# Performance work log

Measured on AMD Instinct MI355X. Metric: run time of the kernel, lower is better.

Reference implementation:

```python
import jax, jax.numpy as jnp
import numpy as np

B_SZ = 4; SEQ = 2048; D_INPUT = 40; D_MODEL = 128; N_LAYERS = 4
D_STATE = 16; EXPAND = 2; D_INNER = D_MODEL * EXPAND
N_HEADS = 4; D_HEAD = D_MODEL // N_HEADS; MAX_LANDMARKS = 100
EPS_RMS = 1.1920929e-07  # torch nn.RMSNorm default eps = finfo(float32).eps
EPS_LN = 1e-5
A_FLOOR = 1e-4


def _rms(x, w):
    return x * jax.lax.rsqrt(jnp.mean(x * x, -1, keepdims=True) + EPS_RMS) * w


def _ln(x, w, b):
    m = jnp.mean(x, -1, keepdims=True)
    v = jnp.mean((x - m) ** 2, -1, keepdims=True)
    return (x - m) * jax.lax.rsqrt(v + EPS_LN) * w + b


def _mamba3_block(xin, Wi, Wx, Wdt, bdt, Alog, Bb, Cb, Bnw, Cnw, rf, Dv, Wo):
    # xin: (B,L,d_model)
    xz = xin @ Wi                       # (B,L,2*d_inner)
    xp, z = jnp.split(xz, 2, axis=-1)
    xp = jax.nn.silu(xp)
    sp = xp @ Wx                        # (B,L,2*d_state+2)
    B_raw = sp[..., :D_STATE]
    C_raw = sp[..., D_STATE:2 * D_STATE]
    dt_in = sp[..., -2:-1]
    lam_in = sp[..., -1:]
    Bm = _rms(B_raw + Bb, Bnw)
    Cm = _rms(C_raw + Cb, Cnw)
    dt = jax.nn.softplus(dt_in @ Wdt + bdt)   # (B,L,d_inner)
    lam = jax.nn.sigmoid(lam_in)              # (B,L,1)
    # data-dependent RoPE on B and C
    freqs = jax.nn.softplus(rf)                                  # (d_state//2,)
    ang = jnp.cumsum(jnp.mean(dt, -1, keepdims=True), axis=1) * freqs  # (B,L,ds/2)
    ca, sa = jnp.cos(ang), jnp.sin(ang)

    def rot(M):
        e, o = M[..., ::2], M[..., 1::2]
        return jnp.stack([e * ca - o * sa, e * sa + o * ca], -1).reshape(M.shape)

    Bm, Cm = rot(Bm), rot(Cm)
    A = jnp.minimum(-jnp.exp(Alog), -A_FLOOR)   # (d_inner,d_state)
    dte = dt[..., None]                          # (B,L,d_inner,1)
    dA = jnp.exp(A * dte)                        # (B,L,d_inner,d_state)
    Bx = Bm[:, :, None, :] * xp[..., None]       # (B,L,d_inner,d_state)
    Bx_prev = jnp.concatenate([jnp.zeros_like(Bx[:, :1]), Bx[:, :-1]], axis=1)
    lame = lam[..., None]                        # (B,L,1,1)
    u = (1.0 - lame) * dte * dA * Bx_prev + lame * dte * Bx
    u = u.at[:, 0].set(dte[:, 0] * Bx[:, 0])     # t==0 case: h = dt*B*x (no lambda)

    def step(h, inp):
        dA_t, u_t, C_t = inp
        h = dA_t * h + u_t
        return h, jnp.sum(h * C_t[:, None, :], -1)

    h0 = jnp.zeros((xin.shape[0], D_INNER, D_STATE), xin.dtype)
    _, ys = jax.lax.scan(step, h0, (jnp.swapaxes(dA, 0, 1), jnp.swapaxes(u, 0, 1), jnp.swapaxes(Cm, 0, 1)))
    y = jnp.swapaxes(ys, 0, 1)                   # (B,L,d_inner)
    y = y + xp * Dv
    y = y * jax.nn.silu(z)
    return y @ Wo


def _landmark_attn(mo, skip, hw, WQ, bQ, WK, bK, WV, bV, WO, bO):
    Bsz, L, Dm = skip.shape
    k = min(MAX_LANDMARKS, L)
    _, idx = jax.lax.top_k(hw, k)
    idx = jnp.sort(idx, axis=1)                            # (B,k)
    kv = jnp.take_along_axis(skip, idx[..., None], axis=1)  # (B,k,Dm)
    q = mo[:, -1:, :]                                       # (B,1,Dm)
    Q = (q @ WQ + bQ).reshape(Bsz, 1, N_HEADS, D_HEAD).transpose(0, 2, 1, 3)
    K = (kv @ WK + bK).reshape(Bsz, k, N_HEADS, D_HEAD).transpose(0, 2, 1, 3)
    V = (kv @ WV + bV).reshape(Bsz, k, N_HEADS, D_HEAD).transpose(0, 2, 1, 3)
    scores = jnp.einsum('bhqd,bhkd->bhqk', Q, K) * (D_HEAD ** -0.5)
    probs = jax.nn.softmax(scores, axis=-1)
    out = jnp.einsum('bhqk,bhkd->bhqd', probs, V).transpose(0, 2, 1, 3).reshape(Bsz, Dm)
    return out @ WO + bO


def setup_inputs() -> dict:
    key = jax.random.key(0)
    ks = iter(jax.random.split(key, 64))

    def nrm(shape, s=0.02):
        return jax.random.normal(next(ks), shape, jnp.float32) * s

    nl, ds, di, dm = N_LAYERS, D_STATE, D_INNER, D_MODEL
    inp = {}
    inp['x'] = jax.random.normal(next(ks), (B_SZ, SEQ, D_INPUT), jnp.float32)
    inp['hawkes_weights'] = jax.random.uniform(next(ks), (B_SZ, SEQ), jnp.float32)
    inp['emb_W'] = nrm((D_INPUT, dm)); inp['emb_b'] = jnp.zeros(dm, jnp.float32)
    inp['skip_W'] = nrm((D_INPUT, dm)); inp['skip_b'] = jnp.zeros(dm, jnp.float32)
    inp['in_proj_W'] = nrm((nl, dm, 2 * di))
    inp['x_proj_W'] = nrm((nl, di, 2 * ds + 2))
    inp['dt_proj_W'] = nrm((nl, 1, di), 1.0)
    inp['dt_proj_b'] = jnp.full((nl, di), -1.0, jnp.float32)
    inp['A_log'] = jnp.broadcast_to(jnp.log(jnp.arange(1, ds + 1, dtype=jnp.float32)), (nl, di, ds)) * jnp.ones((nl, di, ds), jnp.float32)
    inp['B_bias'] = jnp.ones((nl, ds), jnp.float32)
    inp['C_bias'] = jnp.ones((nl, ds), jnp.float32)
    inp['Bn_w'] = jnp.ones((nl, ds), jnp.float32)
    inp['Cn_w'] = jnp.ones((nl, ds), jnp.float32)
    inp['rope_freqs'] = nrm((nl, ds // 2), 0.01)
    inp['D_param'] = jnp.ones((nl, di), jnp.float32)
    inp['out_proj_W'] = nrm((nl, di, dm))
    inp['ln_w'] = jnp.ones((nl, dm), jnp.float32); inp['ln_b'] = jnp.zeros((nl, dm), jnp.float32)
    inp['fn_w'] = jnp.ones(dm, jnp.float32); inp['fn_b'] = jnp.zeros(dm, jnp.float32)
    for nm in ('Q', 'K', 'V', 'O'):
        inp['W' + nm] = nrm((dm, dm)); inp['b' + nm] = jnp.zeros(dm, jnp.float32)
    return inp


def reference(x, hawkes_weights, emb_W, emb_b, skip_W, skip_b, in_proj_W, x_proj_W,
              dt_proj_W, dt_proj_b, A_log, B_bias, C_bias, Bn_w, Cn_w, rope_freqs,
              D_param, out_proj_W, ln_w, ln_b, fn_w, fn_b, WQ, bQ, WK, bK, WV, bV, WO, bO):
    w = hawkes_weights[..., None]
    h = (x @ emb_W + emb_b) * w          # Hawkes-damped embedding for Mamba path
    skip = (x @ skip_W + skip_b) * w     # Hawkes skip for attention KV
    for i in range(N_LAYERS):
        h = h + _mamba3_block(_ln(h, ln_w[i], ln_b[i]), in_proj_W[i], x_proj_W[i],
                              dt_proj_W[i], dt_proj_b[i], A_log[i], B_bias[i], C_bias[i],
                              Bn_w[i], Cn_w[i], rope_freqs[i], D_param[i], out_proj_W[i])
    mo = _ln(h, fn_w, fn_b)
    return _landmark_attn(mo, skip, hawkes_weights, WQ, bQ, WK, bK, WV, bV, WO, bO)
```

## Files before the change

kernel.cpp:

```cpp
#include <hip/hip_runtime.h>
#include <hip/hip_fp16.h>
#include <math.h>

#define BSZ   4
#define SEQL  2048
#define DIN   40
#define DM    128
#define DI    256
#define DS    16
#define NL    4
#define NHEAD 4
#define DHEAD 32
#define KLM   100
#define NC    128
#define TC    16
#define NROWS 8
#define EROWS 16

__device__ __forceinline__ float rcp_(float x){ return __builtin_amdgcn_rcpf(x); }
__device__ __forceinline__ float sigmoidf_(float x){ return rcp_(1.0f + __expf(-x)); }
__device__ __forceinline__ float siluf_(float x){ return x*rcp_(1.0f + __expf(-x)); }
__device__ __forceinline__ float softplusf_(float x){ return fmaxf(x,0.0f) + __logf(1.0f + __expf(-fabsf(x))); }

__device__ __forceinline__ float block_sum256(float v, float* red){
  #pragma unroll
  for (int o=32;o>0;o>>=1) v += __shfl_down(v,o,64);
  __syncthreads();
  if ((threadIdx.x & 63)==0) red[threadIdx.x>>6] = v;
  __syncthreads();
  return red[0]+red[1]+red[2]+red[3];
}
__device__ __forceinline__ void load8(const float* p, float* r){
  const float4* q = (const float4*)p;
  float4 a=q[0], b=q[1];
  r[0]=a.x;r[1]=a.y;r[2]=a.z;r[3]=a.w; r[4]=b.x;r[5]=b.y;r[6]=b.z;r[7]=b.w;
}
__device__ __forceinline__ void store8(float* p, const float* r){
  float4* q = (float4*)p;
  q[0]=make_float4(r[0],r[1],r[2],r[3]);  q[1]=make_float4(r[4],r[5],r[6],r[7]);
}
__device__ __forceinline__ void load16(const float* p, float* r){
  load8(p, r); load8(p+8, r+8);
}
__device__ __forceinline__ void store16(float* p, const float* r){
  store8(p, r); store8(p+8, r+8);
}

__global__ __launch_bounds__(256) void embed_kernel(
    const float* __restrict__ x, const float* __restrict__ hw,
    const float* __restrict__ eW, const float* __restrict__ eb,
    const float* __restrict__ sW, const float* __restrict__ sb,
    float* __restrict__ hb, float* __restrict__ sk)
{
  __shared__ float xr[EROWS][DIN];
  const int t = threadIdx.x;
  const size_t R0 = (size_t)blockIdx.x * EROWS;
  for (int e=t; e<EROWS*DIN; e+=256) ((float*)xr)[e] = x[R0*DIN + e];
  __syncthreads();
  const int c = t & (DM-1), g = t >> 7;
  float ae[8], as[8];
  #pragma unroll
  for (int j=0;j<8;j++){ ae[j]=0.0f; as[j]=0.0f; }
  for (int k=0;k<DIN;k++){
    const float we  = eW[(size_t)k*DM + c];
    const float ws_ = sW[(size_t)k*DM + c];
    #pragma unroll
    for (int j=0;j<8;j++){
      const float xv = xr[g*8+j][k];
      ae[j] = fmaf(xv, we, ae[j]);
      as[j] = fmaf(xv, ws_, as[j]);
    }
  }
  const float ebv = eb[c], sbv = sb[c];
  #pragma unroll
  for (int j=0;j<8;j++){
    const size_t R = R0 + g*8 + j;
    const float w = hw[R];
    hb[R*DM + c] = (ae[j]+ebv)*w;
    sk[R*DM + c] = (as[j]+sbv)*w;
  }
}

__global__ __launch_bounds__(256) void pre_kernel(
    const float* __restrict__ hb,
    const float* __restrict__ Wi, const float* __restrict__ Wx,
    const float* __restrict__ Wdt, const float* __restrict__ bdt,
    const float* __restrict__ Bb, const float* __restrict__ Cb,
    const float* __restrict__ Bnw, const float* __restrict__ Cnw,
    const float* __restrict__ lnw, const float* __restrict__ lnb,
    __half* __restrict__ xph, __half* __restrict__ zsh,
    float* __restrict__ dtin, float* __restrict__ Shalf,
    float* __restrict__ Bmb, float* __restrict__ Cmb,
    float* __restrict__ lamb, float* __restrict__ mdtb)
{
  __shared__ float xin[NROWS][DM+4];
  __shared__ float xps[NROWS][DI+4];
  __shared__ float spl[NROWS][40];
  __shared__ float pr[NROWS][4];

  const int t = threadIdx.x;
  const size_t R0 = (size_t)blockIdx.x * NROWS;

  {
    const int r = t >> 5, j = t & 31;
    const float4 v = ((const float4*)(hb + (R0 + r)*DM))[j];
    float s = v.x+v.y+v.z+v.w;
    #pragma unroll
    for (int o=16;o>0;o>>=1) s += __shfl_xor(s,o,32);
    const float m = s*(1.0f/DM);
    const float dx=v.x-m, dy=v.y-m, dz=v.z-m, dw=v.w-m;
    float ss = dx*dx+dy*dy+dz*dz+dw*dw;
    #pragma unroll
    for (int o=16;o>0;o>>=1) ss += __shfl_xor(ss,o,32);
    const float inv = 1.0f/sqrtf(ss*(1.0f/DM) + 1e-5f);
    const int c = j*4;
    xin[r][c+0] = dx*inv*lnw[c+0] + lnb[c+0];
    xin[r][c+1] = dy*inv*lnw[c+1] + lnb[c+1];
    xin[r][c+2] = dz*inv*lnw[c+2] + lnb[c+2];
    xin[r][c+3] = dw*inv*lnw[c+3] + lnb[c+3];
  }
  __syncthreads();

  {
    float2 a[NROWS];
    #pragma unroll
    for (int r=0;r<NROWS;r++){ a[r].x=0.0f; a[r].y=0.0f; }
    for (int k=0;k<DM;k+=4){
      const float2 w0 = *(const float2*)&Wi[(size_t)(k+0)*(2*DI) + 2*t];
      const float2 w1 = *(const float2*)&Wi[(size_t)(k+1)*(2*DI) + 2*t];
      const float2 w2 = *(const float2*)&Wi[(size_t)(k+2)*(2*DI) + 2*t];
      const float2 w3 = *(const float2*)&Wi[(size_t)(k+3)*(2*DI) + 2*t];
      #pragma unroll
      for (int r=0;r<NROWS;r++){
        const float4 xv = *(const float4*)&xin[r][k];
        a[r].x = fmaf(xv.x,w0.x,a[r].x); a[r].y = fmaf(xv.x,w0.y,a[r].y);
        a[r].x = fmaf(xv.y,w1.x,a[r].x); a[r].y = fmaf(xv.y,w1.y,a[r].y);
        a[r].x = fmaf(xv.z,w2.x,a[r].x); a[r].y = fmaf(xv.z,w2.y,a[r].y);
        a[r].x = fmaf(xv.w,w3.x,a[r].x); a[r].y = fmaf(xv.w,w3.y,a[r].y);
      }
    }
    if (t < 128){
      #pragma unroll
      for (int r=0;r<NROWS;r++){
        const float sx = siluf_(a[r].x), sy = siluf_(a[r].y);
        xps[r][2*t] = sx; xps[r][2*t+1] = sy;
        *(__half2*)&xph[(R0+r)*DI + 2*t] =
            __halves2half2(__float2half_rn(sx), __float2half_rn(sy));
      }
    } else {
      const int zc = 2*t - 2*DI + DI;
      #pragma unroll
      for (int r=0;r<NROWS;r++){
        const float sx = siluf_(a[r].x), sy = siluf_(a[r].y);
        *(__half2*)&zsh[(R0+r)*DI + zc] =
            __halves2half2(__float2half_rn(sx), __float2half_rn(sy));
      }
    }
  }
  __syncthreads();

  if (t < 136){
    const int r = t & 7, op = t >> 3;
    float ax=0.0f, ay=0.0f;
    for (int k=0;k<DI;k+=4){
      const float4 xv = *(const float4*)&xps[r][k];
      const float2 w0 = *(const float2*)&Wx[(size_t)(k+0)*34 + 2*op];
      const float2 w1 = *(const float2*)&Wx[(size_t)(k+1)*34 + 2*op];
      const float2 w2 = *(const float2*)&Wx[(size_t)(k+2)*34 + 2*op];
      const float2 w3 = *(const float2*)&Wx[(size_t)(k+3)*34 + 2*op];
      ax = fmaf(xv.x,w0.x,ax); ay = fmaf(xv.x,w0.y,ay);
      ax = fmaf(xv.y,w1.x,ax); ay = fmaf(xv.y,w1.y,ay);
      ax = fmaf(xv.z,w2.x,ax); ay = fmaf(xv.z,w2.y,ay);
      ax = fmaf(xv.w,w3.x,ax); ay = fmaf(xv.w,w3.y,ay);
    }
    spl[r][2*op] = ax; spl[r][2*op+1] = ay;
  }
  __syncthreads();

  {
    const int half = t >> 7;
    const int r2 = (t >> 4) & 7, s2 = t & 15;
    const float* bias = half ? Cb : Bb;
    const float* wn   = half ? Cnw : Bnw;
    const float v = spl[r2][half*DS + s2] + bias[s2];
    float ss = v*v;
    #pragma unroll
    for (int o=8;o>0;o>>=1) ss += __shfl_xor(ss,o,16);
    const float inv = 1.0f/sqrtf(ss*(1.0f/DS) + 1.1920929e-07f);
    (half ? Cmb : Bmb)[(R0+r2)*DS + s2] = v*inv*wn[s2];
  }

  {
    const int lane = t & 63, w = t >> 6;
    const float wdt = Wdt[t], bdtv = bdt[t];
    float Sd = 0.0f;
    #pragma unroll
    for (int r=0;r<NROWS;r++){
      const float dval = softplusf_(fmaf(spl[r][32], wdt, bdtv));
      Sd += dval;
      float s = dval;
      #pragma unroll
      for (int o=32;o>0;o>>=1) s += __shfl_xor(s,o,64);
      if (lane==0) pr[r][w] = s;
    }
    Shalf[(size_t)blockIdx.x * DI + t] = Sd;
    if (t < NROWS){
      lamb[R0+t] = sigmoidf_(spl[t][33]);
      dtin[R0+t] = spl[t][32];
    }
  }
  __syncthreads();
  if (t < NROWS)
    mdtb[R0+t] = (pr[t][0]+pr[t][1]+pr[t][2]+pr[t][3])*(1.0f/DI);
}

__global__ __launch_bounds__(256) void cumsum_kernel(
    const float* __restrict__ mdt, double* __restrict__ csum_g)
{
  __shared__ double wsum[4];
  const int b = blockIdx.x, t = threadIdx.x;
  const int lane = t & 63, w = t >> 6;
  const float* p = mdt + (size_t)b*SEQL + (size_t)t*8;
  double v[8]; double s = 0.0;
  #pragma unroll
  for (int q=0;q<8;q++){ v[q] = (double)p[q]; s += v[q]; }
  double sc = s;
  #pragma unroll
  for (int o=1;o<64;o<<=1){
    const double nb = __shfl_up(sc, o, 64);
    if (lane >= o) sc += nb;
  }
  if (lane==63) wsum[w] = sc;
  __syncthreads();
  double woff = 0.0;
  for (int j=0;j<w;j++) woff += wsum[j];
  double run = woff + sc - s;
  double* dst = csum_g + (size_t)b*SEQL + (size_t)t*8;
  #pragma unroll
  for (int q=0;q<8;q++){ run += v[q]; dst[q] = run; }
}

__global__ __launch_bounds__(256) void csfill_kernel(
    const double* __restrict__ csum_g, const float* __restrict__ rf,
    float2* __restrict__ cst)
{
  __shared__ double fqs[8];
  const int t = threadIdx.x;
  if (t < 8){
    const double xfr = (double)rf[t];
    fqs[t] = fmax(xfr, 0.0) + log1p(exp(-fabs(xfr)));
  }
  __syncthreads();
  const int row = blockIdx.x*256 + t;
  const double ab = csum_g[row];
  const double TWO_PI = 6.283185307179586;
  const double INV2PI = 0.15915494309189535;
  float2 o8[8];
  #pragma unroll
  for (int f=0; f<8; f++){
    const double ang = ab * fqs[f];
    const double red = ang - floor(ang*INV2PI)*TWO_PI;
    float sa, ca;
    __sincosf((float)red, &sa, &ca);
    o8[f] = make_float2(ca, sa);
  }
  float4* dst = (float4*)&cst[(size_t)row*8];
  dst[0] = make_float4(o8[0].x,o8[0].y,o8[1].x,o8[1].y);
  dst[1] = make_float4(o8[2].x,o8[2].y,o8[3].x,o8[3].y);
  dst[2] = make_float4(o8[4].x,o8[4].y,o8[5].x,o8[5].y);
  dst[3] = make_float4(o8[6].x,o8[6].y,o8[7].x,o8[7].y);
}

__global__ __launch_bounds__(512) void scan1_kernel(
    const __half* __restrict__ xph, const float* __restrict__ dtin,
    const float* __restrict__ Wdt, const float* __restrict__ bdt,
    const float* __restrict__ Bmb, const float* __restrict__ lamb,
    const float2* __restrict__ cst,
    const float* __restrict__ Alog, float* __restrict__ hend)
{
  __shared__ float Bst[TC+1][DS];
  __shared__ float lst[TC];
  __shared__ float dsl[TC];
  __shared__ __half xpl[TC+1][DI+8];
  const int t = threadIdx.x;
  const int d  = t >> 1;
  const int s0 = (t & 1) * 8;
  const int c = blockIdx.x & (NC-1);
  const int b = blockIdx.x >> 7;
  const size_t bL = (size_t)b*SEQL;
  const int t0 = c*TC;
  const int id = blockIdx.x*256 + d;

  for (int e=t; e<(TC+1)*DS; e+=512){
    const int j = e >> 4, s = e & 15;
    const int trow = t0 - 1 + j;
    Bst[j][s] = (trow >= 0) ? Bmb[(bL + trow)*DS + s] : 0.0f;
  }
  for (int e=t; e<(TC+1)*DI; e+=512){
    const int j = e >> 8, dd = e & (DI-1);
    const int trow = t0 - 1 + j;
    xpl[j][dd] = (trow >= 0) ? xph[(bL + trow)*DI + dd] : __float2half_rn(0.0f);
  }
  if (t < TC){
    lst[t] = lamb[bL + t0 + t];
    dsl[t] = dtin[bL + t0 + t];
  }
  __syncthreads();
  if (t < 136){
    const int j = t >> 3, f = t & 7;
    const int trow = t0 - 1 + j;
    if (trow >= 0){
      const float2 cs = cst[((size_t)(bL + trow))*8 + f];
      const float e0 = Bst[j][2*f], o0 = Bst[j][2*f+1];
      Bst[j][2*f]   = e0*cs.x - o0*cs.y;
      Bst[j][2*f+1] = e0*cs.y + o0*cs.x;
    }
  }
  __syncthreads();

  float A[8];
  #pragma unroll
  for (int s=0;s<8;s++) A[s] = fminf(-__expf(Alog[d*DS + s0 + s]), -1e-4f);
  const float wdt = Wdt[d], bdtv = bdt[d];
  float h[8], Bprev[8];
  #pragma unroll
  for (int s=0;s<8;s++) h[s]=0.0f;
  float xpm1;
  int tstart;
  if (t0 > 0){
    #pragma unroll
    for (int s=0;s<8;s++) Bprev[s] = Bst[0][s0+s];
    xpm1 = __half2float(xpl[0][d]);
    tstart = t0;
  } else {
    const float dtv = softplusf_(fmaf(dsl[0], wdt, bdtv));
    const float xpv = __half2float(xpl[1][d]);
    #pragma unroll
    for (int s=0;s<8;s++){
      h[s] = dtv*(Bst[1][s0+s]*xpv);
      Bprev[s] = Bst[1][s0+s];
    }
    xpm1 = xpv;
    tstart = 1;
  }
  for (int tt=tstart; tt<t0+TC; ++tt){
    const int j = tt - t0;
    const float dtv = softplusf_(fmaf(dsl[j], wdt, bdtv));
    const float xpv = __half2float(xpl[j+1][d]);
    const float lamv = lst[j];
    const float dl = dtv*lamv;
    const float dml = dtv - dl;
    #pragma unroll
    for (int s=0;s<8;s++){
      const float a = __expf(A[s]*dtv);
      const float Bc = Bst[j+1][s0+s];
      const float u = fmaf(dml*a, Bprev[s]*xpm1, dl*(Bc*xpv));
      h[s] = fmaf(a, h[s], u);
      Bprev[s] = Bc;
    }
    xpm1 = xpv;
  }
  store8(hend + (size_t)id*DS + s0, h);
}

__global__ __launch_bounds__(128) void scan2_kernel(
    float* __restrict__ hend, const float* __restrict__ Shalf,
    const float* __restrict__ Alog)
{
  __shared__ float hS[NC][DS+1];
  __shared__ float pS[NC][DS+1];
  const int c = threadIdx.x;
  const int d = blockIdx.x & (DI-1);
  const int b = blockIdx.x >> 8;
  const float S = Shalf[(size_t)(b*(SEQL/NROWS) + 2*c)*DI + d]
                + Shalf[(size_t)(b*(SEQL/NROWS) + 2*c + 1)*DI + d];
  float P[DS], h[DS];
  #pragma unroll
  for (int s=0;s<DS;s++){
    const float A = fminf(-__expf(Alog[d*DS+s]), -1e-4f);
    P[s] = __expf(A*S);
  }
  load16(hend + (((size_t)(b*NC + c))*DI + d)*DS, h);
  #pragma unroll
  for (int s=0;s<DS;s++){ hS[c][s]=h[s]; pS[c][s]=P[s]; }
  __syncthreads();
  for (int off=1; off<NC; off<<=1){
    float hn[DS], pn[DS];
    const int src = c - off;
    if (src >= 0){
      #pragma unroll
      for (int s=0;s<DS;s++){ hn[s]=hS[src][s]; pn[s]=pS[src][s]; }
    }
    __syncthreads();
    if (src >= 0){
      #pragma unroll
      for (int s=0;s<DS;s++){
        h[s] = fmaf(P[s], hn[s], h[s]);
        P[s] *= pn[s];
        hS[c][s] = h[s]; pS[c][s] = P[s];
      }
    }
    __syncthreads();
  }
  float o[DS];
  if (c == 0){
    #pragma unroll
    for (int s=0;s<DS;s++) o[s] = 0.0f;
  } else {
    #pragma unroll
    for (int s=0;s<DS;s++) o[s] = hS[c-1][s];
  }
  store16(hend + (((size_t)(b*NC + c))*DI + d)*DS, o);
}

__global__ __launch_bounds__(512) void scan3post_kernel(
    const __half* __restrict__ xph, const float* __restrict__ dtin,
    const float* __restrict__ Wdt, const float* __restrict__ bdt,
    const float* __restrict__ Bmb, const float* __restrict__ Cmb,
    const float* __restrict__ lamb, const __half* __restrict__ zsh,
    const float2* __restrict__ cst,
    const float* __restrict__ Alog, const float* __restrict__ Dv,
    const float* __restrict__ Hin, const float* __restrict__ Wo,
    float* __restrict__ hb)
{
  __shared__ float Bst[TC+1][DS];
  __shared__ float Cst[TC][DS];
  __shared__ float lst[TC];
  __shared__ float dsl[TC];
  __shared__ __half xpl[TC+1][DI+8];
  __shared__ __half zsl[TC][DI+8];
  __shared__ float ys[TC][DI+4];
  const int t = threadIdx.x;
  const int d  = t >> 1;
  const int sh = t & 1;
  const int s0 = sh * 8;
  const int c = blockIdx.x & (NC-1);
  const int b = blockIdx.x >> 7;
  const size_t bL = (size_t)b*SEQL;
  const int t0 = c*TC;
  const int id = blockIdx.x*256 + d;

  for (int e=t; e<(TC+1)*DS; e+=512){
    const int j = e >> 4, s = e & 15;
    const int trow = t0 - 1 + j;
    Bst[j][s] = (trow >= 0) ? Bmb[(bL + trow)*DS + s] : 0.0f;
    if (j < TC) Cst[j][s] = Cmb[(bL + t0 + j)*DS + s];
  }
  for (int e=t; e<(TC+1)*DI; e+=512){
    const int j = e >> 8, dd = e & (DI-1);
    const int trow = t0 - 1 + j;
    xpl[j][dd] = (trow >= 0) ? xph[(bL + trow)*DI + dd] : __float2half_rn(0.0f);
    if (j < TC) zsl[j][dd] = zsh[(bL + t0 + j)*DI + dd];
  }
  if (t < TC){
    lst[t] = lamb[bL + t0 + t];
    dsl[t] = dtin[bL + t0 + t];
  }
  __syncthreads();
  if (t < 264){
    if (t < 136){
      const int j = t >> 3, f = t & 7;
      const int trow = t0 - 1 + j;
      if (trow >= 0){
        const float2 cs = cst[((size_t)(bL + trow))*8 + f];
        const float e0 = Bst[j][2*f], o0 = Bst[j][2*f+1];
        Bst[j][2*f]   = e0*cs.x - o0*cs.y;
        Bst[j][2*f+1] = e0*cs.y + o0*cs.x;
      }
    } else {
      const int e2 = t - 136;
      const int j = e2 >> 3, f = e2 & 7;
      const float2 cs = cst[((size_t)(bL + t0 + j))*8 + f];
      const float e0 = Cst[j][2*f], o0 = Cst[j][2*f+1];
      Cst[j][2*f]   = e0*cs.x - o0*cs.y;
      Cst[j][2*f+1] = e0*cs.y + o0*cs.x;
    }
  }
  __syncthreads();

  float A[8];
  #pragma unroll
  for (int s=0;s<8;s++) A[s] = fminf(-__expf(Alog[d*DS + s0 + s]), -1e-4f);
  const float wdt = Wdt[d], bdtv = bdt[d];
  const float dvp = Dv[d];
  float h[8], Bprev[8];
  load8(Hin + (size_t)id*DS + s0, h);
  float xpm1;
  int tstart;
  if (t0 > 0){
    #pragma unroll
    for (int s=0;s<8;s++) Bprev[s] = Bst[0][s0+s];
    xpm1 = __half2float(xpl[0][d]);
    tstart = t0;
  } else {
    const float dtv = softplusf_(fmaf(dsl[0], wdt, bdtv));
    const float xpv = __half2float(xpl[1][d]);
    float y = 0.0f;
    #pragma unroll
    for (int s=0;s<8;s++){
      h[s] = dtv*(Bst[1][s0+s]*xpv);
      y = fmaf(h[s], Cst[0][s0+s], y);
      Bprev[s] = Bst[1][s0+s];
    }
    const float ytot = y + __shfl_xor(y, 1, 64);
    if (sh == 0) ys[0][d] = (ytot + xpv*dvp)*__half2float(zsl[0][d]);
    xpm1 = xpv;
    tstart = 1;
  }
  for (int tt=tstart; tt<t0+TC; ++tt){
    const int j = tt - t0;
    const float dtv = softplusf_(fmaf(dsl[j], wdt, bdtv));
    const float xpv = __half2float(xpl[j+1][d]);
    const float lamv = lst[j];
    const float dl = dtv*lamv;
    const float dml = dtv - dl;
    float y = 0.0f;
    #pragma unroll
    for (int s=0;s<8;s++){
      const float a = __expf(A[s]*dtv);
      const float Bc = Bst[j+1][s0+s];
      const float u = fmaf(dml*a, Bprev[s]*xpm1, dl*(Bc*xpv));
      h[s] = fmaf(a, h[s], u);
      y = fmaf(h[s], Cst[j][s0+s], y);
      Bprev[s] = Bc;
    }
    const float ytot = y + __shfl_xor(y, 1, 64);
    if (sh == 0) ys[j][d] = (ytot + xpv*dvp)*__half2float(zsl[j][d]);
    xpm1 = xpv;
  }
  __syncthreads();

  {
    const int r  = t >> 5;
    const int cg = t & 31;
    const int c0 = cg*4;
    float acc[4] = {0.0f,0.0f,0.0f,0.0f};
    for (int k=0;k<DI;k+=4){
      const float4 yv = *(const float4*)&ys[r][k];
      const float yy[4] = {yv.x, yv.y, yv.z, yv.w};
      #pragma unroll
      for (int j=0;j<4;j++){
        const float4 wa = *(const float4*)&Wo[(size_t)(k+j)*DM + c0];
        acc[0]=fmaf(yy[j],wa.x,acc[0]); acc[1]=fmaf(yy[j],wa.y,acc[1]);
        acc[2]=fmaf(yy[j],wa.z,acc[2]); acc[3]=fmaf(yy[j],wa.w,acc[3]);
      }
    }
    const size_t row = bL + t0 + r;
    float4 h0 = *(const float4*)&hb[row*DM + c0];
    h0.x+=acc[0]; h0.y+=acc[1]; h0.z+=acc[2]; h0.w+=acc[3];
    *(float4*)&hb[row*DM + c0] = h0;
  }
}

__global__ __launch_bounds__(256) void topk_kernel(
    const float* __restrict__ hb, const float* __restrict__ hw,
    const float* __restrict__ fnw, const float* __restrict__ fnb,
    int* __restrict__ idxl_g, float* __restrict__ mog)
{
  __shared__ int redcnt[2][4];
  __shared__ int eqc[8][4], gtc[8][4];
  __shared__ float red_f[4];

  const int b = blockIdx.x;
  const int t = threadIdx.x;
  const int lane = t & 63, w = t >> 6;

  const float* hwp = hw + (size_t)b*SEQL;
  unsigned vb[8];
  #pragma unroll
  for (int q=0;q<8;q++) vb[q] = __float_as_uint(hwp[q*256 + t]);

  unsigned kth = 0u;
  for (int bit=31; bit>=0; --bit){
    const unsigned cand = kth | (1u << bit);
    int c0 = 0;
    #pragma unroll
    for (int q=0;q<8;q++) c0 += __popcll(__ballot(vb[q] >= cand));
    const int par = bit & 1;
    if (lane == 0) redcnt[par][w] = c0;
    __syncthreads();
    const int tot = redcnt[par][0]+redcnt[par][1]+redcnt[par][2]+redcnt[par][3];
    if (tot >= KLM) kth = cand;
  }

  unsigned long long beq[8], bgt[8];
  #pragma unroll
  for (int q=0;q<8;q++){
    beq[q] = __ballot(vb[q] == kth);
    bgt[q] = __ballot(vb[q] >  kth);
  }
  if (lane == 0){
    #pragma unroll
    for (int q=0;q<8;q++){ eqc[q][w] = __popcll(beq[q]); gtc[q][w] = __popcll(bgt[q]); }
  }
  __syncthreads();
  {
    int gtTot = 0;
    #pragma unroll
    for (int q=0;q<8;q++) gtTot += gtc[q][0]+gtc[q][1]+gtc[q][2]+gtc[q][3];
    const int need_eq = KLM - gtTot;
    const unsigned long long lmask = (lane==0) ? 0ull : ((~0ull) >> (64-lane));
    int eqPfx = 0, gtPfx = 0;
    #pragma unroll
    for (int q=0;q<8;q++){
      int eqWP = 0, gtWP = 0;
      for (int w2=0; w2<w; ++w2){ eqWP += eqc[q][w2]; gtWP += gtc[q][w2]; }
      const int eqBefore = eqPfx + eqWP + __popcll(beq[q] & lmask);
      const int gtBefore = gtPfx + gtWP + __popcll(bgt[q] & lmask);
      if (vb[q] > kth){
        const int pos = gtBefore + min(eqBefore, need_eq);
        if (pos < KLM) idxl_g[b*KLM + pos] = q*256 + t;
      } else if (vb[q] == kth && eqBefore < need_eq){
        const int pos = gtBefore + eqBefore;
        if (pos < KLM) idxl_g[b*KLM + pos] = q*256 + t;
      }
      eqPfx += eqc[q][0]+eqc[q][1]+eqc[q][2]+eqc[q][3];
      gtPfx += gtc[q][0]+gtc[q][1]+gtc[q][2]+gtc[q][3];
    }
  }

  {
    const float* hr = hb + ((size_t)b*SEQL + (SEQL-1))*DM;
    const float hv = (t < DM) ? hr[t] : 0.0f;
    const float ssum = block_sum256(hv, red_f);
    const float mean = ssum*(1.0f/DM);
    const float dv = (t < DM) ? (hv - mean) : 0.0f;
    const float vsum = block_sum256(dv*dv, red_f);
    const float inv = 1.0f/sqrtf(vsum*(1.0f/DM) + 1e-5f);
    if (t < DM) mog[b*DM + t] = dv*inv*fnw[t] + fnb[t];
  }
}

__global__ __launch_bounds__(256) void attnmid_kernel(
    const float* __restrict__ sk, const int* __restrict__ idxl_g,
    const float* __restrict__ mog,
    const float* __restrict__ WQ, const float* __restrict__ bQ,
    const float* __restrict__ WK, const float* __restrict__ bK,
    const float* __restrict__ WV, const float* __restrict__ bV,
    float* __restrict__ attnog)
{
  __shared__ float kv[KLM][DM+4];
  __shared__ float Qs[DHEAD];
  __shared__ float qk[DM];
  __shared__ float sc[KLM];
  __shared__ float pbar[DM];
  __shared__ float bterm_s;
  const int t = threadIdx.x;
  const int b = blockIdx.x >> 2, hh = blockIdx.x & 3;
  const int c0 = hh*DHEAD;

  for (int e=t; e<KLM*DM; e+=256){
    const int j = e >> 7, cc = e & (DM-1);
    kv[j][cc] = sk[((size_t)b*SEQL + idxl_g[b*KLM + j])*DM + cc];
  }
  if (t < DHEAD){
    float a = bQ[c0+t];
    #pragma unroll 4
    for (int k=0;k<DM;k++) a = fmaf(mog[b*DM+k], WQ[(size_t)k*DM + c0+t], a);
    Qs[t] = a;
  }
  __syncthreads();
  if (t < DM){
    float a = 0.0f;
    #pragma unroll
    for (int cc=0; cc<DHEAD; cc++) a = fmaf(WK[(size_t)t*DM + c0 + cc], Qs[cc], a);
    qk[t] = a;
  } else if (t == DM){
    float a = 0.0f;
    for (int cc=0; cc<DHEAD; cc++) a += bK[c0+cc]*Qs[cc];
    bterm_s = a;
  }
  __syncthreads();
  if (t < KLM){
    float a = bterm_s;
    for (int m=0;m<DM;m+=4){
      const float4 kvv = *(const float4*)&kv[t][m];
      const float4 qv  = *(const float4*)&qk[m];
      a = fmaf(kvv.x,qv.x,a); a = fmaf(kvv.y,qv.y,a);
      a = fmaf(kvv.z,qv.z,a); a = fmaf(kvv.w,qv.w,a);
    }
    sc[t] = a*0.17677669529663687f;
  }
  __syncthreads();
  if (t < 64){
    const int lane = t;
    const float v0 = (lane < KLM) ? sc[lane] : -3.0e38f;
    const float v1 = (lane+64 < KLM) ? sc[lane+64] : -3.0e38f;
    float mx = fmaxf(v0, v1);
    #pragma unroll
    for (int o2=32;o2>0;o2>>=1) mx = fmaxf(mx, __shfl_xor(mx,o2,64));
    const float e0 = (lane < KLM) ? __expf(v0-mx) : 0.0f;
    const float e1 = (lane+64 < KLM) ? __expf(v1-mx) : 0.0f;
    float sm = e0+e1;
    #pragma unroll
    for (int o2=32;o2>0;o2>>=1) sm += __shfl_xor(sm,o2,64);
    const float inv2 = rcp_(sm);
    if (lane < KLM) sc[lane] = e0*inv2;
    if (lane+64 < KLM) sc[lane+64] = e1*inv2;
  }
  __syncthreads();
  if (t < DM){
    float a = 0.0f;
    #pragma unroll 4
    for (int j=0;j<KLM;j++) a = fmaf(sc[j], kv[j][t], a);
    pbar[t] = a;
  }
  __syncthreads();
  if (t < DHEAD){
    const int cc = c0 + t;
    float a = bV[cc];
    #pragma unroll 4
    for (int m=0;m<DM;m++) a = fmaf(pbar[m], WV[(size_t)m*DM + cc], a);
    attnog[b*DM + cc] = a;
  }
}

__global__ __launch_bounds__(128) void attnout_kernel(
    const float* __restrict__ attnog, const float* __restrict__ WO,
    const float* __restrict__ bO, float* __restrict__ outp)
{
  __shared__ float ao[DM];
  const int b = blockIdx.x, t = threadIdx.x;
  ao[t] = attnog[b*DM + t];
  __syncthreads();
  float a = bO[t];
  #pragma unroll 4
  for (int c2=0;c2<DM;c2++) a = fmaf(ao[c2], WO[(size_t)c2*DM + t], a);
  outp[(size_t)b*DM + t] = a;
}

extern "C" void kernel_launch(void* const* d_in, const int* in_sizes, int n_in,
                              void* d_out, int out_size, void* d_ws, size_t ws_size,
                              hipStream_t stream)
{
  (void)in_sizes; (void)n_in; (void)out_size; (void)ws_size;
  const float* x    = (const float*)d_in[0];
  const float* hw   = (const float*)d_in[1];
  const float* embW = (const float*)d_in[2];
  const float* embB = (const float*)d_in[3];
  const float* skW  = (const float*)d_in[4];
  const float* skB  = (const float*)d_in[5];
  const float* inW  = (const float*)d_in[6];
  const float* xpW  = (const float*)d_in[7];
  const float* dtW  = (const float*)d_in[8];
  const float* dtB  = (const float*)d_in[9];
  const float* Alog = (const float*)d_in[10];
  const float* Bb   = (const float*)d_in[11];
  const float* Cb   = (const float*)d_in[12];
  const float* Bnw  = (const float*)d_in[13];
  const float* Cnw  = (const float*)d_in[14];
  const float* rf   = (const float*)d_in[15];
  const float* Dpar = (const float*)d_in[16];
  const float* outW = (const float*)d_in[17];
  const float* lnW  = (const float*)d_in[18];
  const float* lnB  = (const float*)d_in[19];
  const float* fnW  = (const float*)d_in[20];
  const float* fnB  = (const float*)d_in[21];
  const float* WQ = (const float*)d_in[22]; const float* bQ = (const float*)d_in[23];
  const float* WK = (const float*)d_in[24]; const float* bK = (const float*)d_in[25];
  const float* WV = (const float*)d_in[26]; const float* bV = (const float*)d_in[27];
  const float* WO = (const float*)d_in[28]; const float* bO = (const float*)d_in[29];

  float* ws = (float*)d_ws;
  size_t off = 0;
  float* hb    = ws + off; off += (size_t)BSZ*SEQL*DM;
  float* sk    = ws + off; off += (size_t)BSZ*SEQL*DM;
  __half* xph  = (__half*)(ws + off); off += (size_t)BSZ*SEQL*DI/2;
  __half* zsh  = (__half*)(ws + off); off += (size_t)BSZ*SEQL*DI/2;
  float* Bmb   = ws + off; off += (size_t)BSZ*SEQL*DS;
  float* Cmb   = ws + off; off += (size_t)BSZ*SEQL*DS;
  float* lamb  = ws + off; off += (size_t)BSZ*SEQL;
  float* mdtb  = ws + off; off += (size_t)BSZ*SEQL;
  float* dtin  = ws + off; off += (size_t)BSZ*SEQL;
  float* Shalf = ws + off; off += (size_t)BSZ*(SEQL/NROWS)*DI;
  float* hend  = ws + off; off += (size_t)BSZ*NC*DI*DS;
  float2* cst  = (float2*)(ws + off); off += (size_t)BSZ*SEQL*16;
  double* csum_g = (double*)(ws + off); off += (size_t)BSZ*SEQL*2;
  int* idxl_g  = (int*)(ws + off); off += (size_t)BSZ*KLM;
  float* mog   = ws + off; off += (size_t)BSZ*DM;
  float* attnog= ws + off; off += (size_t)BSZ*DM;

  embed_kernel<<<BSZ*SEQL/EROWS, 256, 0, stream>>>(x, hw, embW, embB, skW, skB, hb, sk);

  for (int i=0;i<NL;i++){
    pre_kernel<<<BSZ*SEQL/NROWS, 256, 0, stream>>>(hb,
        inW + (size_t)i*DM*2*DI, xpW + (size_t)i*DI*34,
        dtW + (size_t)i*DI, dtB + (size_t)i*DI,
        Bb + i*DS, Cb + i*DS, Bnw + i*DS, Cnw + i*DS,
        lnW + i*DM, lnB + i*DM,
        xph, zsh, dtin, Shalf, Bmb, Cmb, lamb, mdtb);
    cumsum_kernel<<<BSZ, 256, 0, stream>>>(mdtb, csum_g);
    csfill_kernel<<<BSZ*SEQL/256, 256, 0, stream>>>(csum_g, rf + i*8, cst);
    scan1_kernel<<<BSZ*NC, 512, 0, stream>>>(xph, dtin,
        dtW + (size_t)i*DI, dtB + (size_t)i*DI,
        Bmb, lamb, cst, Alog + (size_t)i*DI*DS, hend);
    scan2_kernel<<<BSZ*DI, 128, 0, stream>>>(hend, Shalf, Alog + (size_t)i*DI*DS);
    scan3post_kernel<<<BSZ*NC, 512, 0, stream>>>(xph, dtin,
        dtW + (size_t)i*DI, dtB + (size_t)i*DI,
        Bmb, Cmb, lamb, zsh, cst,
        Alog + (size_t)i*DI*DS, Dpar + (size_t)i*DI, hend,
        outW + (size_t)i*DI*DM, hb);
  }

  topk_kernel<<<BSZ, 256, 0, stream>>>(hb, hw, fnW, fnB, idxl_g, mog);
  attnmid_kernel<<<BSZ*NHEAD, 256, 0, stream>>>(sk, idxl_g, mog,
      WQ, bQ, WK, bK, WV, bV, attnog);
  attnout_kernel<<<BSZ, 128, 0, stream>>>(attnog, WO, bO, (float*)d_out);
}
```

Before: 576.3 us.

## Fuse chunked scan passes into one cooperative kernel with grid syncs

```diff
diff --git a/kernel.cpp b/kernel.cpp
--- a/kernel.cpp
+++ b/kernel.cpp
@@ -1,6 +1,9 @@
 #include <hip/hip_runtime.h>
 #include <hip/hip_fp16.h>
+#include <hip/hip_cooperative_groups.h>
 #include <math.h>
+
+namespace cg = cooperative_groups;
 
 #define BSZ   4
 #define SEQL  2048
@@ -38,12 +41,6 @@
 __device__ __forceinline__ void store8(float* p, const float* r){
   float4* q = (float4*)p;
   q[0]=make_float4(r[0],r[1],r[2],r[3]);  q[1]=make_float4(r[4],r[5],r[6],r[7]);
-}
-__device__ __forceinline__ void load16(const float* p, float* r){
-  load8(p, r); load8(p+8, r+8);
-}
-__device__ __forceinline__ void store16(float* p, const float* r){
-  store8(p, r); store8(p+8, r+8);
 }
 
 __global__ __launch_bounds__(256) void embed_kernel(
@@ -271,157 +268,15 @@
   dst[3] = make_float4(o8[6].x,o8[6].y,o8[7].x,o8[7].y);
 }
 
-__global__ __launch_bounds__(512) void scan1_kernel(
-    const __half* __restrict__ xph, const float* __restrict__ dtin,
-    const float* __restrict__ Wdt, const float* __restrict__ bdt,
-    const float* __restrict__ Bmb, const float* __restrict__ lamb,
-    const float2* __restrict__ cst,
-    const float* __restrict__ Alog, float* __restrict__ hend)
-{
-  __shared__ float Bst[TC+1][DS];
-  __shared__ float lst[TC];
-  __shared__ float dsl[TC];
-  __shared__ __half xpl[TC+1][DI+8];
-  const int t = threadIdx.x;
-  const int d  = t >> 1;
-  const int s0 = (t & 1) * 8;
-  const int c = blockIdx.x & (NC-1);
-  const int b = blockIdx.x >> 7;
-  const size_t bL = (size_t)b*SEQL;
-  const int t0 = c*TC;
-  const int id = blockIdx.x*256 + d;
-
-  for (int e=t; e<(TC+1)*DS; e+=512){
-    const int j = e >> 4, s = e & 15;
-    const int trow = t0 - 1 + j;
-    Bst[j][s] = (trow >= 0) ? Bmb[(bL + trow)*DS + s] : 0.0f;
-  }
-  for (int e=t; e<(TC+1)*DI; e+=512){
-    const int j = e >> 8, dd = e & (DI-1);
-    const int trow = t0 - 1 + j;
-    xpl[j][dd] = (trow >= 0) ? xph[(bL + trow)*DI + dd] : __float2half_rn(0.0f);
-  }
-  if (t < TC){
-    lst[t] = lamb[bL + t0 + t];
-    dsl[t] = dtin[bL + t0 + t];
-  }
-  __syncthreads();
-  if (t < 136){
-    const int j = t >> 3, f = t & 7;
-    const int trow = t0 - 1 + j;
-    if (trow >= 0){
-      const float2 cs = cst[((size_t)(bL + trow))*8 + f];
-      const float e0 = Bst[j][2*f], o0 = Bst[j][2*f+1];
-      Bst[j][2*f]   = e0*cs.x - o0*cs.y;
-      Bst[j][2*f+1] = e0*cs.y + o0*cs.x;
-    }
-  }
-  __syncthreads();
-
-  float A[8];
-  #pragma unroll
-  for (int s=0;s<8;s++) A[s] = fminf(-__expf(Alog[d*DS + s0 + s]), -1e-4f);
-  const float wdt = Wdt[d], bdtv = bdt[d];
-  float h[8], Bprev[8];
-  #pragma unroll
-  for (int s=0;s<8;s++) h[s]=0.0f;
-  float xpm1;
-  int tstart;
-  if (t0 > 0){
-    #pragma unroll
-    for (int s=0;s<8;s++) Bprev[s] = Bst[0][s0+s];
-    xpm1 = __half2float(xpl[0][d]);
-    tstart = t0;
-  } else {
-    const float dtv = softplusf_(fmaf(dsl[0], wdt, bdtv));
-    const float xpv = __half2float(xpl[1][d]);
-    #pragma unroll
-    for (int s=0;s<8;s++){
-      h[s] = dtv*(Bst[1][s0+s]*xpv);
-      Bprev[s] = Bst[1][s0+s];
-    }
-    xpm1 = xpv;
-    tstart = 1;
-  }
-  for (int tt=tstart; tt<t0+TC; ++tt){
-    const int j = tt - t0;
-    const float dtv = softplusf_(fmaf(dsl[j], wdt, bdtv));
-    const float xpv = __half2float(xpl[j+1][d]);
-    const float lamv = lst[j];
-    const float dl = dtv*lamv;
-    const float dml = dtv - dl;
-    #pragma unroll
-    for (int s=0;s<8;s++){
-      const float a = __expf(A[s]*dtv);
-      const float Bc = Bst[j+1][s0+s];
-      const float u = fmaf(dml*a, Bprev[s]*xpm1, dl*(Bc*xpv));
-      h[s] = fmaf(a, h[s], u);
-      Bprev[s] = Bc;
-    }
-    xpm1 = xpv;
-  }
-  store8(hend + (size_t)id*DS + s0, h);
-}
-
-__global__ __launch_bounds__(128) void scan2_kernel(
-    float* __restrict__ hend, const float* __restrict__ Shalf,
-    const float* __restrict__ Alog)
-{
-  __shared__ float hS[NC][DS+1];
-  __shared__ float pS[NC][DS+1];
-  const int c = threadIdx.x;
-  const int d = blockIdx.x & (DI-1);
-  const int b = blockIdx.x >> 8;
-  const float S = Shalf[(size_t)(b*(SEQL/NROWS) + 2*c)*DI + d]
-                + Shalf[(size_t)(b*(SEQL/NROWS) + 2*c + 1)*DI + d];
-  float P[DS], h[DS];
-  #pragma unroll
-  for (int s=0;s<DS;s++){
-    const float A = fminf(-__expf(Alog[d*DS+s]), -1e-4f);
-    P[s] = __expf(A*S);
-  }
-  load16(hend + (((size_t)(b*NC + c))*DI + d)*DS, h);
-  #pragma unroll
-  for (int s=0;s<DS;s++){ hS[c][s]=h[s]; pS[c][s]=P[s]; }
-  __syncthreads();
-  for (int off=1; off<NC; off<<=1){
-    float hn[DS], pn[DS];
-    const int src = c - off;
-    if (src >= 0){
-      #pragma unroll
-      for (int s=0;s<DS;s++){ hn[s]=hS[src][s]; pn[s]=pS[src][s]; }
-    }
-    __syncthreads();
-    if (src >= 0){
-      #pragma unroll
-      for (int s=0;s<DS;s++){
-        h[s] = fmaf(P[s], hn[s], h[s]);
-        P[s] *= pn[s];
-        hS[c][s] = h[s]; pS[c][s] = P[s];
-      }
-    }
-    __syncthreads();
-  }
-  float o[DS];
-  if (c == 0){
-    #pragma unroll
-    for (int s=0;s<DS;s++) o[s] = 0.0f;
-  } else {
-    #pragma unroll
-    for (int s=0;s<DS;s++) o[s] = hS[c-1][s];
-  }
-  store16(hend + (((size_t)(b*NC + c))*DI + d)*DS, o);
-}
-
-__global__ __launch_bounds__(512) void scan3post_kernel(
+__global__ __launch_bounds__(512, 4) void scan_all_kernel(
     const __half* __restrict__ xph, const float* __restrict__ dtin,
     const float* __restrict__ Wdt, const float* __restrict__ bdt,
     const float* __restrict__ Bmb, const float* __restrict__ Cmb,
     const float* __restrict__ lamb, const __half* __restrict__ zsh,
     const float2* __restrict__ cst,
     const float* __restrict__ Alog, const float* __restrict__ Dv,
-    const float* __restrict__ Hin, const float* __restrict__ Wo,
-    float* __restrict__ hb)
+    const float* __restrict__ Shalf, float* __restrict__ hend,
+    const float* __restrict__ Wo, float* __restrict__ hb)
 {
   __shared__ float Bst[TC+1][DS];
   __shared__ float Cst[TC][DS];
@@ -430,6 +285,7 @@
   __shared__ __half xpl[TC+1][DI+8];
   __shared__ __half zsl[TC][DI+8];
   __shared__ float ys[TC][DI+4];
+
   const int t = threadIdx.x;
   const int d  = t >> 1;
   const int sh = t & 1;
@@ -482,73 +338,207 @@
   #pragma unroll
   for (int s=0;s<8;s++) A[s] = fminf(-__expf(Alog[d*DS + s0 + s]), -1e-4f);
   const float wdt = Wdt[d], bdtv = bdt[d];
-  const float dvp = Dv[d];
-  float h[8], Bprev[8];
-  load8(Hin + (size_t)id*DS + s0, h);
-  float xpm1;
-  int tstart;
-  if (t0 > 0){
-    #pragma unroll
-    for (int s=0;s<8;s++) Bprev[s] = Bst[0][s0+s];
-    xpm1 = __half2float(xpl[0][d]);
-    tstart = t0;
-  } else {
-    const float dtv = softplusf_(fmaf(dsl[0], wdt, bdtv));
-    const float xpv = __half2float(xpl[1][d]);
-    float y = 0.0f;
-    #pragma unroll
-    for (int s=0;s<8;s++){
-      h[s] = dtv*(Bst[1][s0+s]*xpv);
-      y = fmaf(h[s], Cst[0][s0+s], y);
-      Bprev[s] = Bst[1][s0+s];
-    }
-    const float ytot = y + __shfl_xor(y, 1, 64);
-    if (sh == 0) ys[0][d] = (ytot + xpv*dvp)*__half2float(zsl[0][d]);
-    xpm1 = xpv;
-    tstart = 1;
-  }
-  for (int tt=tstart; tt<t0+TC; ++tt){
-    const int j = tt - t0;
-    const float dtv = softplusf_(fmaf(dsl[j], wdt, bdtv));
-    const float xpv = __half2float(xpl[j+1][d]);
-    const float lamv = lst[j];
-    const float dl = dtv*lamv;
-    const float dml = dtv - dl;
-    float y = 0.0f;
-    #pragma unroll
-    for (int s=0;s<8;s++){
-      const float a = __expf(A[s]*dtv);
-      const float Bc = Bst[j+1][s0+s];
-      const float u = fmaf(dml*a, Bprev[s]*xpm1, dl*(Bc*xpv));
-      h[s] = fmaf(a, h[s], u);
-      y = fmaf(h[s], Cst[j][s0+s], y);
-      Bprev[s] = Bc;
-    }
-    const float ytot = y + __shfl_xor(y, 1, 64);
-    if (sh == 0) ys[j][d] = (ytot + xpv*dvp)*__half2float(zsl[j][d]);
-    xpm1 = xpv;
-  }
-  __syncthreads();
-
-  {
-    const int r  = t >> 5;
-    const int cg = t & 31;
-    const int c0 = cg*4;
-    float acc[4] = {0.0f,0.0f,0.0f,0.0f};
-    for (int k=0;k<DI;k+=4){
-      const float4 yv = *(const float4*)&ys[r][k];
-      const float yy[4] = {yv.x, yv.y, yv.z, yv.w};
+
+  {
+    float h[8], Bprev[8];
+    #pragma unroll
+    for (int s=0;s<8;s++) h[s]=0.0f;
+    float xpm1;
+    int tstart;
+    if (t0 > 0){
+      #pragma unroll
+      for (int s=0;s<8;s++) Bprev[s] = Bst[0][s0+s];
+      xpm1 = __half2float(xpl[0][d]);
+      tstart = 0;
+    } else {
+      const float dtv = softplusf_(fmaf(dsl[0], wdt, bdtv));
+      const float xpv = __half2float(xpl[1][d]);
+      #pragma unroll
+      for (int s=0;s<8;s++){
+        h[s] = dtv*(Bst[1][s0+s]*xpv);
+        Bprev[s] = Bst[1][s0+s];
+      }
+      xpm1 = xpv;
+      tstart = 1;
+    }
+    for (int j=tstart; j<TC; ++j){
+      const float dtv = softplusf_(fmaf(dsl[j], wdt, bdtv));
+      const float xpv = __half2float(xpl[j+1][d]);
+      const float lamv = lst[j];
+      const float dl = dtv*lamv;
+      const float dml = dtv - dl;
+      #pragma unroll
+      for (int s=0;s<8;s++){
+        const float a = __expf(A[s]*dtv);
+        const float Bc = Bst[j+1][s0+s];
+        const float u = fmaf(dml*a, Bprev[s]*xpm1, dl*(Bc*xpv));
+        h[s] = fmaf(a, h[s], u);
+        Bprev[s] = Bc;
+      }
+      xpm1 = xpv;
+    }
+    store8(hend + (size_t)id*DS + s0, h);
+  }
+  __threadfence();
+  cg::this_grid().sync();
+
+  {
+    const int wg = t >> 6, lane = t & 63;
+    if (wg < 4){
+      const int g = blockIdx.x*4 + wg;
+      const int gb = g >> 9, gd = (g >> 1) & 255, gsh = g & 1;
+      const int gs0 = gsh*8;
+      float A2[8];
+      #pragma unroll
+      for (int s=0;s<8;s++) A2[s] = fminf(-__expf(Alog[gd*DS + gs0 + s]), -1e-4f);
+      const int c0 = 2*lane, c1 = 2*lane + 1;
+      float h0[8], h1[8];
+      load8(hend + (((size_t)(gb*NC + c0))*DI + gd)*DS + gs0, h0);
+      load8(hend + (((size_t)(gb*NC + c1))*DI + gd)*DS + gs0, h1);
+      const float S0 = Shalf[((size_t)gb*256 + 2*c0)*DI + gd]
+                     + Shalf[((size_t)gb*256 + 2*c0 + 1)*DI + gd];
+      const float S1 = Shalf[((size_t)gb*256 + 2*c1)*DI + gd]
+                     + Shalf[((size_t)gb*256 + 2*c1 + 1)*DI + gd];
+      float P0[8], hC[8], PC[8];
+      #pragma unroll
+      for (int s=0;s<8;s++){
+        P0[s] = __expf(A2[s]*S0);
+        const float P1 = __expf(A2[s]*S1);
+        hC[s] = fmaf(P1, h0[s], h1[s]);
+        PC[s] = P1*P0[s];
+      }
+      #pragma unroll
+      for (int off=1; off<64; off<<=1){
+        float hp[8], pp[8];
+        #pragma unroll
+        for (int s=0;s<8;s++){ hp[s] = __shfl_up(hC[s], off, 64); pp[s] = __shfl_up(PC[s], off, 64); }
+        if (lane >= off){
+          #pragma unroll
+          for (int s=0;s<8;s++){ hC[s] = fmaf(PC[s], hp[s], hC[s]); PC[s] *= pp[s]; }
+        }
+      }
+      float hx[8];
+      #pragma unroll
+      for (int s=0;s<8;s++){
+        const float v = __shfl_up(hC[s], 1, 64);
+        hx[s] = (lane == 0) ? 0.0f : v;
+      }
+      store8(hend + (((size_t)(gb*NC + c0))*DI + gd)*DS + gs0, hx);
+      float hx1[8];
+      #pragma unroll
+      for (int s=0;s<8;s++) hx1[s] = fmaf(P0[s], hx[s], h0[s]);
+      store8(hend + (((size_t)(gb*NC + c1))*DI + gd)*DS + gs0, hx1);
+    }
+  }
+  __threadfence();
+  cg::this_grid().sync();
+
+  {
+    const float dvp = Dv[d];
+    float h[8], Bprev[8];
+    load8(hend + (size_t)id*DS + s0, h);
+    float xpm1;
+    int tstart;
+    if (t0 > 0){
+      #pragma unroll
+      for (int s=0;s<8;s++) Bprev[s] = Bst[0][s0+s];
+      xpm1 = __half2float(xpl[0][d]);
+      tstart = 0;
+    } else {
+      const float dtv = softplusf_(fmaf(dsl[0], wdt, bdtv));
+      const float xpv = __half2float(xpl[1][d]);
+      float y = 0.0f;
+      #pragma unroll
+      for (int s=0;s<8;s++){
+        h[s] = dtv*(Bst[1][s0+s]*xpv);
+        y = fmaf(h[s], Cst[0][s0+s], y);
+        Bprev[s] = Bst[1][s0+s];
+      }
+      const float ytot = y + __shfl_xor(y, 1, 64);
+      if (sh == 0) ys[0][d] = (ytot + xpv*dvp)*__half2float(zsl[0][d]);
+      xpm1 = xpv;
+      tstart = 1;
+    }
+    for (int j=tstart; j<TC; ++j){
+      const float dtv = softplusf_(fmaf(dsl[j], wdt, bdtv));
+      const float xpv = __half2float(xpl[j+1][d]);
+      const float lamv = lst[j];
+      const float dl = dtv*lamv;
+      const float dml = dtv - dl;
+      float y = 0.0f;
+      #pragma unroll
+      for (int s=0;s<8;s++){
+        const float a = __expf(A[s]*dtv);
+        const float Bc = Bst[j+1][s0+s];
+        const float u = fmaf(dml*a, Bprev[s]*xpm1, dl*(Bc*xpv));
+        h[s] = fmaf(a, h[s], u);
+        y = fmaf(h[s], Cst[j][s0+s], y);
+        Bprev[s] = Bc;
+      }
+      const float ytot = y + __shfl_xor(y, 1, 64);
+      if (sh == 0) ys[j][d] = (ytot + xpv*dvp)*__half2float(zsl[j][d]);
+      xpm1 = xpv;
+    }
+  }
+  __syncthreads();
+
+  {
+    const int cg2  = t & 31;
+    const int ks2  = (t >> 5) & 1;
+    const int rg   = (t >> 6) & 3;
+    const int ksHi = t >> 8;
+    const int seg = ksHi*2 + ks2;
+    const int k0 = seg*64;
+    const int c0c = cg2*4;
+    float acc[4][4];
+    #pragma unroll
+    for (int rr=0;rr<4;rr++){ acc[rr][0]=0.f; acc[rr][1]=0.f; acc[rr][2]=0.f; acc[rr][3]=0.f; }
+    for (int k=k0; k<k0+64; k+=4){
+      float4 yv[4];
+      #pragma unroll
+      for (int rr=0;rr<4;rr++) yv[rr] = *(const float4*)&ys[rg*4+rr][k];
       #pragma unroll
       for (int j=0;j<4;j++){
-        const float4 wa = *(const float4*)&Wo[(size_t)(k+j)*DM + c0];
-        acc[0]=fmaf(yy[j],wa.x,acc[0]); acc[1]=fmaf(yy[j],wa.y,acc[1]);
-        acc[2]=fmaf(yy[j],wa.z,acc[2]); acc[3]=fmaf(yy[j],wa.w,acc[3]);
-      }
-    }
-    const size_t row = bL + t0 + r;
-    float4 h0 = *(const float4*)&hb[row*DM + c0];
-    h0.x+=acc[0]; h0.y+=acc[1]; h0.z+=acc[2]; h0.w+=acc[3];
-    *(float4*)&hb[row*DM + c0] = h0;
+        const float4 wv = *(const float4*)&Wo[(size_t)(k+j)*DM + c0c];
+        const float y0 = (j==0)?yv[0].x:(j==1)?yv[0].y:(j==2)?yv[0].z:yv[0].w;
+        const float y1 = (j==0)?yv[1].x:(j==1)?yv[1].y:(j==2)?yv[1].z:yv[1].w;
+        const float y2 = (j==0)?yv[2].x:(j==1)?yv[2].y:(j==2)?yv[2].z:yv[2].w;
+        const float y3 = (j==0)?yv[3].x:(j==1)?yv[3].y:(j==2)?yv[3].z:yv[3].w;
+        acc[0][0]=fmaf(y0,wv.x,acc[0][0]); acc[0][1]=fmaf(y0,wv.y,acc[0][1]);
+        acc[0][2]=fmaf(y0,wv.z,acc[0][2]); acc[0][3]=fmaf(y0,wv.w,acc[0][3]);
+        acc[1][0]=fmaf(y1,wv.x,acc[1][0]); acc[1][1]=fmaf(y1,wv.y,acc[1][1]);
+        acc[1][2]=fmaf(y1,wv.z,acc[1][2]); acc[1][3]=fmaf(y1,wv.w,acc[1][3]);
+        acc[2][0]=fmaf(y2,wv.x,acc[2][0]); acc[2][1]=fmaf(y2,wv.y,acc[2][1]);
+        acc[2][2]=fmaf(y2,wv.z,acc[2][2]); acc[2][3]=fmaf(y2,wv.w,acc[2][3]);
+        acc[3][0]=fmaf(y3,wv.x,acc[3][0]); acc[3][1]=fmaf(y3,wv.y,acc[3][1]);
+        acc[3][2]=fmaf(y3,wv.z,acc[3][2]); acc[3][3]=fmaf(y3,wv.w,acc[3][3]);
+      }
+    }
+    #pragma unroll
+    for (int rr=0;rr<4;rr++){
+      #pragma unroll
+      for (int cc=0;cc<4;cc++) acc[rr][cc] += __shfl_down(acc[rr][cc], 32, 64);
+    }
+    float (*red)[132] = (float(*)[132])ys;
+    __syncthreads();
+    const int lane = t & 63;
+    if (ksHi == 1 && lane < 32){
+      #pragma unroll
+      for (int rr=0;rr<4;rr++)
+        *(float4*)&red[rg*4+rr][c0c] = make_float4(acc[rr][0],acc[rr][1],acc[rr][2],acc[rr][3]);
+    }
+    __syncthreads();
+    if (ksHi == 0 && lane < 32){
+      #pragma unroll
+      for (int rr=0;rr<4;rr++){
+        const float4 rv = *(const float4*)&red[rg*4+rr][c0c];
+        const size_t row = bL + t0 + rg*4 + rr;
+        float4 hv = *(const float4*)&hb[row*DM + c0c];
+        hv.x += acc[rr][0] + rv.x; hv.y += acc[rr][1] + rv.y;
+        hv.z += acc[rr][2] + rv.z; hv.w += acc[rr][3] + rv.w;
+        *(float4*)&hb[row*DM + c0c] = hv;
+      }
+    }
   }
 }
 
@@ -791,15 +781,27 @@
         xph, zsh, dtin, Shalf, Bmb, Cmb, lamb, mdtb);
     cumsum_kernel<<<BSZ, 256, 0, stream>>>(mdtb, csum_g);
     csfill_kernel<<<BSZ*SEQL/256, 256, 0, stream>>>(csum_g, rf + i*8, cst);
-    scan1_kernel<<<BSZ*NC, 512, 0, stream>>>(xph, dtin,
-        dtW + (size_t)i*DI, dtB + (size_t)i*DI,
-        Bmb, lamb, cst, Alog + (size_t)i*DI*DS, hend);
-    scan2_kernel<<<BSZ*DI, 128, 0, stream>>>(hend, Shalf, Alog + (size_t)i*DI*DS);
-    scan3post_kernel<<<BSZ*NC, 512, 0, stream>>>(xph, dtin,
-        dtW + (size_t)i*DI, dtB + (size_t)i*DI,
-        Bmb, Cmb, lamb, zsh, cst,
-        Alog + (size_t)i*DI*DS, Dpar + (size_t)i*DI, hend,
-        outW + (size_t)i*DI*DM, hb);
+
+    const __half* xph_c = xph; const float* dtin_c = dtin;
+    const float* Wdt_i = dtW + (size_t)i*DI;
+    const float* bdt_i = dtB + (size_t)i*DI;
+    const float* Bmb_c = Bmb; const float* Cmb_c = Cmb;
+    const float* lamb_c = lamb; const __half* zsh_c = zsh;
+    const float2* cst_c = cst;
+    const float* Alog_i = Alog + (size_t)i*DI*DS;
+    const float* Dv_i = Dpar + (size_t)i*DI;
+    const float* Shalf_c = Shalf;
+    float* hend_m = hend;
+    const float* Wo_i = outW + (size_t)i*DI*DM;
+    float* hb_m = hb;
+    void* args[] = {
+      (void*)&xph_c, (void*)&dtin_c, (void*)&Wdt_i, (void*)&bdt_i,
+      (void*)&Bmb_c, (void*)&Cmb_c, (void*)&lamb_c, (void*)&zsh_c,
+      (void*)&cst_c, (void*)&Alog_i, (void*)&Dv_i, (void*)&Shalf_c,
+      (void*)&hend_m, (void*)&Wo_i, (void*)&hb_m
+    };
+    hipLaunchCooperativeKernel((const void*)scan_all_kernel,
+        dim3(BSZ*NC), dim3(512), args, 0, stream);
   }
 
   topk_kernel<<<BSZ, 256, 0, stream>>>(hb, hw, fnW, fnB, idxl_g, mog);
```

Measured after the change: 1.728 ms. 3x slower.
